# Performance work log

Hardware: AMD Instinct MI355X
Metric: run time of the kernel (lower is better)

Reference implementation:

```python
import jax, jax.numpy as jnp
import numpy as np

B, NP, P, DIM = 128, 64, 128, 512
DST, DCONV, DEPTH = 16, 4, 2
DIN = 2 * DIM          # expand * dim
DTR = DIM // 16        # dt_rank
NCLS = 32


def setup_inputs() -> dict:
    key = jax.random.key(0)
    ks = jax.random.split(key, 12)
    r = lambda k, shape, s=0.02: jax.random.normal(k, shape, jnp.float32) * s
    A_log = jnp.log(jnp.arange(1, DST + 1, dtype=jnp.float32))  # S4D-real init
    return {
        "series": jax.random.normal(ks[0], (B, NP * P), jnp.float32),
        "seg_w": r(ks[1], (NP, P, DIM)),
        "seg_b": jnp.zeros((NP, DIM), jnp.float32),
        "ln_g": jnp.ones((NP, DIM), jnp.float32),
        "ln_b": jnp.zeros((NP, DIM), jnp.float32),
        "in_proj_w": r(ks[2], (DEPTH, 2 * DIN, DIM)),
        "conv_w": r(ks[3], (DEPTH, DIN, DCONV), 0.1),
        "conv_b": jnp.zeros((DEPTH, DIN), jnp.float32),
        "x_proj_w": r(ks[4], (DEPTH, DTR + 2 * DST, DIN)),
        "dt_proj_w": r(ks[5], (DEPTH, DIN, DTR), 0.1),
        "dt_proj_b": r(ks[6], (DEPTH, DIN), 0.5) - 4.0,  # small softplus(dt)
        "A_log": jnp.tile(A_log, (DEPTH, DIN, 1)),
        "D": jnp.ones((DEPTH, DIN), jnp.float32),
        "out_proj_w": r(ks[7], (DEPTH, DIM, DIN)),
        "head_ln_g": jnp.ones((NP * DIM,), jnp.float32),
        "head_ln_b": jnp.zeros((NP * DIM,), jnp.float32),
        "head_w": r(ks[8], (NCLS, NP * DIM)),
        "head_b": jnp.zeros((NCLS,), jnp.float32),
    }


def _layernorm(x, g, b, eps=1e-5):
    mu = x.mean(-1, keepdims=True)
    var = x.var(-1, keepdims=True)
    return (x - mu) / jnp.sqrt(var + eps) * g + b


def _mamba_block(x, wi, cw, cb, wx, wdt, bdt, A_log, Dp, wo):
    # x: [b, l, DIM]
    b, l, _ = x.shape
    xz = jnp.einsum('bld,ed->ble', x, wi)            # [b, l, 2*DIN]
    u, z = jnp.split(xz, 2, axis=-1)
    # depthwise causal conv1d (kernel DCONV, left pad DCONV-1)
    up = jnp.pad(u, ((0, 0), (DCONV - 1, 0), (0, 0)))
    uc = sum(up[:, k:k + l, :] * cw[:, k] for k in range(DCONV)) + cb
    uc = jax.nn.silu(uc)
    x_dbl = jnp.einsum('bld,ed->ble', uc, wx)        # [b, l, DTR+2*DST]
    dt, Bm, Cm = jnp.split(x_dbl, [DTR, DTR + DST], axis=-1)
    delta = jax.nn.softplus(jnp.einsum('blr,dr->bld', dt, wdt) + bdt)  # [b,l,DIN]
    A = -jnp.exp(A_log)                               # [DIN, DST]

    def step(h, inp):
        d_t, B_t, C_t, u_t = inp                      # [b,DIN],[b,DST],[b,DST],[b,DIN]
        dA = jnp.exp(d_t[:, :, None] * A)             # [b, DIN, DST]
        h = dA * h + (d_t * u_t)[:, :, None] * B_t[:, None, :]
        y = jnp.einsum('bdn,bn->bd', h, C_t)
        return h, y

    xs = (delta.transpose(1, 0, 2), Bm.transpose(1, 0, 2),
          Cm.transpose(1, 0, 2), uc.transpose(1, 0, 2))
    h0 = jnp.zeros((b, DIN, DST), x.dtype)
    _, ys = jax.lax.scan(step, h0, xs)                # [l, b, DIN]
    y = ys.transpose(1, 0, 2) + uc * Dp
    y = y * jax.nn.silu(z)
    return jnp.einsum('bld,ed->ble', y, wo)           # [b, l, DIM]


def _forward(series, seg_w, seg_b, ln_g, ln_b, in_proj_w, conv_w, conv_b,
             x_proj_w, dt_proj_w, dt_proj_b, A_log, D, out_proj_w,
             head_ln_g, head_ln_b, head_w, head_b):
    b = series.shape[0]
    x = series.reshape(b, NP, P)                      # equal-size pathway split
    x = jnp.einsum('bnp,npd->bnd', x, seg_w) + seg_b  # per-pathway Linear
    x = _layernorm(x, ln_g, ln_b)                     # per-pathway LayerNorm
    for i in range(DEPTH):                            # stacked Mamba (no residual)
        x = _mamba_block(x, in_proj_w[i], conv_w[i], conv_b[i], x_proj_w[i],
                         dt_proj_w[i], dt_proj_b[i], A_log[i], D[i], out_proj_w[i])
    x = x.reshape(b, NP * DIM)
    x = _layernorm(x, head_ln_g, head_ln_b)
    return x @ head_w.T + head_b


def reference(series, seg_w, seg_b, ln_g, ln_b, in_proj_w, conv_w, conv_b,
              x_proj_w, dt_proj_w, dt_proj_b, A_log, D, out_proj_w,
              head_ln_g, head_ln_b, head_w, head_b):
    return _forward(series, seg_w, seg_b, ln_g, ln_b, in_proj_w, conv_w, conv_b,
                    x_proj_w, dt_proj_w, dt_proj_b, A_log, D, out_proj_w,
                    head_ln_g, head_ln_b, head_w, head_b)
```

## Files before the change

### kernel.cpp

```cpp
#include <hip/hip_runtime.h>

typedef unsigned short u16;
typedef unsigned int   u32;
typedef __attribute__((ext_vector_type(8))) short short8;
typedef __attribute__((ext_vector_type(4))) float floatx4;

static __device__ __forceinline__ float silu_f(float x){
  return x / (1.f + __expf(-x));
}
static __device__ __forceinline__ float bfu2f(u16 u){
  union { u32 i; float f; } v; v.i = ((u32)u) << 16; return v.f;
}
static __device__ __forceinline__ u16 f2bfu(float f){
  union { float f; u32 i; } v; v.f = f;
  u32 x = v.i;
  u32 r = (x + 0x7fffu + ((x >> 16) & 1u)) >> 16;
  return (u16)r;
}
static __device__ __forceinline__ float softplus_f(float v){
  return fmaxf(v, 0.f) + log1pf(__expf(-fabsf(v)));
}

constexpr int cB = 128, cNP = 64, cP = 128, cDIM = 512, cDIN = 1024;
constexpr int cDST = 16, cDTR = 32, cNCLS = 32;
constexpr int cBL = cB * cNP;
constexpr int cXZ = 2 * cDIN;

__global__ __launch_bounds__(256) void k_f2bf(
    const float* __restrict__ src, u16* __restrict__ dst)
{
  const int i = (blockIdx.x * 256 + threadIdx.x) * 4;
  float4 v = *(const float4*)(src + i);
  ushort4 o;
  o.x = f2bfu(v.x); o.y = f2bfu(v.y); o.z = f2bfu(v.z); o.w = f2bfu(v.w);
  *(ushort4*)(dst + i) = o;
}

__global__ __launch_bounds__(256) void k_segT(
    const float* __restrict__ src, u16* __restrict__ dst)
{
  const int n = blockIdx.z;
  const int p0 = blockIdx.x * 32;
  const int d0 = blockIdx.y * 32;
  const int tx = threadIdx.x & 31;
  const int ty = threadIdx.x >> 5;
  __shared__ float t[32][33];
#pragma unroll
  for (int r = 0; r < 4; ++r)
    t[ty + r * 8][tx] = src[(size_t)n * (cP * cDIM) + (p0 + ty + r * 8) * cDIM + d0 + tx];
  __syncthreads();
#pragma unroll
  for (int r = 0; r < 4; ++r)
    dst[(size_t)n * (cDIM * cP) + (d0 + ty + r * 8) * cP + p0 + tx] =
        f2bfu(t[tx][ty + r * 8]);
}

template<bool AF32, int EPI>
__global__ __launch_bounds__(256) void k_gemm_mfma(
    const void* __restrict__ Av, int lda,
    const u16* __restrict__ W,
    float* __restrict__ C, int ldc,
    u16* __restrict__ Cb, int ldcb,
    const float* __restrict__ bias,
    int K, long azs, long wzs, long czs,
    const float* __restrict__ cwp, const float* __restrict__ cbp,
    u16* __restrict__ ucp)
{
  constexpr int LDT = 40;
  __shared__ __align__(16) u16 As[128 * LDT];
  __shared__ __align__(16) u16 Ws[128 * LDT];
  __shared__ __align__(16) u16 sU[(EPI == 2) ? 128 * 128 : 1];

  const int bz = blockIdx.z;
  const u16* Wz = W + (size_t)bz * wzs;

  const int tid = threadIdx.x;
  const int bm = blockIdx.x * 128;
  const int bn = blockIdx.y * 128;
  const int wave = tid >> 6;
  const int lane = tid & 63;
  const int wm = (wave & 1) * 64;
  const int wn = (wave >> 1) * 64;
  const int l15 = lane & 15;
  const int quad = lane >> 4;

  floatx4 acc[4][4];
#pragma unroll
  for (int i = 0; i < 4; ++i)
#pragma unroll
    for (int j = 0; j < 4; ++j) acc[i][j] = (floatx4){0.f, 0.f, 0.f, 0.f};

  const int r0 = tid >> 2;
  const int c0 = (tid & 3) * 8;

  const float* Af = (const float*)Av + (AF32 ? (size_t)bz * azs : 0);
  const u16*   Ab = (const u16*)Av + (AF32 ? 0 : (size_t)bz * azs);

  float4 fa0, fb0, fa1, fb1;
  short8 ra0, ra1, rw0, rw1;

  if constexpr (AF32) {
    const float* p0 = Af + (size_t)(bm + r0) * lda + c0;
    const float* p1 = Af + (size_t)(bm + r0 + 64) * lda + c0;
    fa0 = *(const float4*)p0; fb0 = *(const float4*)(p0 + 4);
    fa1 = *(const float4*)p1; fb1 = *(const float4*)(p1 + 4);
  } else {
    ra0 = *(const short8*)(Ab + (size_t)(bm + r0)      * lda + c0);
    ra1 = *(const short8*)(Ab + (size_t)(bm + r0 + 64) * lda + c0);
  }
  rw0 = *(const short8*)(Wz + (size_t)(bn + r0)      * K + c0);
  rw1 = *(const short8*)(Wz + (size_t)(bn + r0 + 64) * K + c0);

  for (int k0 = 0; k0 < K; k0 += 32) {
    if constexpr (AF32) {
      short8 s0, s1;
      s0[0] = (short)f2bfu(fa0.x); s0[1] = (short)f2bfu(fa0.y);
      s0[2] = (short)f2bfu(fa0.z); s0[3] = (short)f2bfu(fa0.w);
      s0[4] = (short)f2bfu(fb0.x); s0[5] = (short)f2bfu(fb0.y);
      s0[6] = (short)f2bfu(fb0.z); s0[7] = (short)f2bfu(fb0.w);
      s1[0] = (short)f2bfu(fa1.x); s1[1] = (short)f2bfu(fa1.y);
      s1[2] = (short)f2bfu(fa1.z); s1[3] = (short)f2bfu(fa1.w);
      s1[4] = (short)f2bfu(fb1.x); s1[5] = (short)f2bfu(fb1.y);
      s1[6] = (short)f2bfu(fb1.z); s1[7] = (short)f2bfu(fb1.w);
      *(short8*)&As[r0 * LDT + c0] = s0;
      *(short8*)&As[(r0 + 64) * LDT + c0] = s1;
    } else {
      *(short8*)&As[r0 * LDT + c0] = ra0;
      *(short8*)&As[(r0 + 64) * LDT + c0] = ra1;
    }
    *(short8*)&Ws[r0 * LDT + c0] = rw0;
    *(short8*)&Ws[(r0 + 64) * LDT + c0] = rw1;
    __syncthreads();

    const int kn = k0 + 32;
    if (kn < K) {
      if constexpr (AF32) {
        const float* p0 = Af + (size_t)(bm + r0) * lda + kn + c0;
        const float* p1 = Af + (size_t)(bm + r0 + 64) * lda + kn + c0;
        fa0 = *(const float4*)p0; fb0 = *(const float4*)(p0 + 4);
        fa1 = *(const float4*)p1; fb1 = *(const float4*)(p1 + 4);
      } else {
        ra0 = *(const short8*)(Ab + (size_t)(bm + r0)      * lda + kn + c0);
        ra1 = *(const short8*)(Ab + (size_t)(bm + r0 + 64) * lda + kn + c0);
      }
      rw0 = *(const short8*)(Wz + (size_t)(bn + r0)      * K + kn + c0);
      rw1 = *(const short8*)(Wz + (size_t)(bn + r0 + 64) * K + kn + c0);
    }

    short8 af[4], bf[4];
#pragma unroll
    for (int i = 0; i < 4; ++i)
      af[i] = *(const short8*)&As[(wm + i * 16 + l15) * LDT + quad * 8];
#pragma unroll
    for (int j = 0; j < 4; ++j)
      bf[j] = *(const short8*)&Ws[(wn + j * 16 + l15) * LDT + quad * 8];
#pragma unroll
    for (int i = 0; i < 4; ++i)
#pragma unroll
      for (int j = 0; j < 4; ++j)
        acc[i][j] = __builtin_amdgcn_mfma_f32_16x16x32_bf16(
            af[i], bf[j], acc[i][j], 0, 0, 0);
    __syncthreads();
  }

  if constexpr (EPI == 2) {
    if (bn < cDIN) {
#pragma unroll
      for (int i = 0; i < 4; ++i) {
        const int mi = wm + i * 16 + quad * 4;
#pragma unroll
        for (int j = 0; j < 4; ++j) {
          const int nj = wn + j * 16 + l15;
#pragma unroll
          for (int r = 0; r < 4; ++r)
            sU[(mi + r) * 128 + nj] = f2bfu(acc[i][j][r]);
        }
      }
      __syncthreads();
      const int c = tid & 127;
      const int s = tid >> 7;
      const int b = (bm >> 6) + s;
      const int d = bn + c;
      const float w0 = cwp[d * 4 + 0], w1 = cwp[d * 4 + 1];
      const float w2 = cwp[d * 4 + 2], w3 = cwp[d * 4 + 3];
      const float cbias = cbp[d];
      u16* dst = ucp + (size_t)b * cNP * cDIN + d;
      float u0 = 0.f, u1 = 0.f, u2 = 0.f;
#pragma unroll 8
      for (int l = 0; l < cNP; ++l) {
        float u3 = bfu2f(sU[(s * 64 + l) * 128 + c]);
        float v = w0 * u0 + w1 * u1 + w2 * u2 + w3 * u3 + cbias;
        dst[(size_t)l * cDIN] = f2bfu(silu_f(v));
        u0 = u1; u1 = u2; u2 = u3;
      }
      return;
    }
  }

#pragma unroll
  for (int i = 0; i < 4; ++i) {
    const int m0 = bm + wm + i * 16 + quad * 4;
#pragma unroll
    for (int j = 0; j < 4; ++j) {
      const int n = bn + wn + j * 16 + l15;
      if constexpr (EPI == 1) {
        const float bs = bias[n];
#pragma unroll
        for (int r = 0; r < 4; ++r)
          Cb[(size_t)(m0 + r) * ldcb + n + bz * czs] =
              f2bfu(softplus_f(acc[i][j][r] + bs));
      } else {
        if (C) {
#pragma unroll
          for (int r = 0; r < 4; ++r)
            C[(size_t)(m0 + r) * ldc + n + bz * czs] = acc[i][j][r];
        }
        if (Cb) {
#pragma unroll
          for (int r = 0; r < 4; ++r)
            Cb[(size_t)(m0 + r) * ldcb + n + bz * czs] = f2bfu(acc[i][j][r]);
        }
      }
    }
  }
}

__global__ __launch_bounds__(256) void k_ln(
    const float* __restrict__ xs, const float* __restrict__ sb,
    const float* __restrict__ ln_g, const float* __restrict__ ln_b,
    u16* __restrict__ x0b)
{
  const int tid = threadIdx.x;
  const int r = blockIdx.x * 4 + (tid >> 6);
  const int lane = tid & 63;
  const int d = lane * 8;
  const int n = r & 63;

  const float* row = xs + (size_t)r * cDIM + d;
  float4 a = *(const float4*)row;
  float4 b = *(const float4*)(row + 4);
  const float* sbp = sb + n * cDIM + d;
  float4 s0 = *(const float4*)sbp;
  float4 s1 = *(const float4*)(sbp + 4);
  a.x += s0.x; a.y += s0.y; a.z += s0.z; a.w += s0.w;
  b.x += s1.x; b.y += s1.y; b.z += s1.z; b.w += s1.w;

  float s  = a.x + a.y + a.z + a.w + b.x + b.y + b.z + b.w;
  float s2 = a.x*a.x + a.y*a.y + a.z*a.z + a.w*a.w
           + b.x*b.x + b.y*b.y + b.z*b.z + b.w*b.w;
#pragma unroll
  for (int m = 1; m < 64; m <<= 1) {
    s  += __shfl_xor(s,  m, 64);
    s2 += __shfl_xor(s2, m, 64);
  }
  const float mu = s * (1.f / cDIM);
  const float var = s2 * (1.f / cDIM) - mu * mu;
  const float rstd = rsqrtf(var + 1e-5f);

  const float* g = ln_g + n * cDIM + d;
  const float* be = ln_b + n * cDIM + d;
  float4 g0 = *(const float4*)g, g1 = *(const float4*)(g + 4);
  float4 b0 = *(const float4*)be, b1 = *(const float4*)(be + 4);
  ushort4 o0, o1;
  o0.x = f2bfu((a.x - mu) * rstd * g0.x + b0.x);
  o0.y = f2bfu((a.y - mu) * rstd * g0.y + b0.y);
  o0.z = f2bfu((a.z - mu) * rstd * g0.z + b0.z);
  o0.w = f2bfu((a.w - mu) * rstd * g0.w + b0.w);
  o1.x = f2bfu((b.x - mu) * rstd * g1.x + b1.x);
  o1.y = f2bfu((b.y - mu) * rstd * g1.y + b1.y);
  o1.z = f2bfu((b.z - mu) * rstd * g1.z + b1.z);
  o1.w = f2bfu((b.w - mu) * rstd * g1.w + b1.w);
  *(ushort4*)(x0b + (size_t)r * cDIM + d) = o0;
  *(ushort4*)(x0b + (size_t)r * cDIM + d + 4) = o1;
}

__global__ __launch_bounds__(128) void k_xproj(
    const u16* __restrict__ A, const u16* __restrict__ W,
    float* __restrict__ xpart)
{
  constexpr int LDT = 40;
  __shared__ __align__(16) u16 As[128 * LDT];
  __shared__ __align__(16) u16 Ws[64 * LDT];

  const int tid = threadIdx.x;
  const int bm = blockIdx.x * 128;
  const int kbase = blockIdx.y * 256;
  const int wave = tid >> 6;
  const int lane = tid & 63;
  const int wm = wave * 64;
  const int l15 = lane & 15;
  const int quad = lane >> 4;

  floatx4 acc[4][4];
#pragma unroll
  for (int i = 0; i < 4; ++i)
#pragma unroll
    for (int j = 0; j < 4; ++j) acc[i][j] = (floatx4){0.f, 0.f, 0.f, 0.f};

  short8 rA[4], rW[2];
#pragma unroll
  for (int it = 0; it < 4; ++it) {
    int idx = tid + it * 128, row = idx >> 2, cc = (idx & 3) * 8;
    rA[it] = *(const short8*)(A + (size_t)(bm + row) * cDIN + kbase + cc);
  }
#pragma unroll
  for (int it = 0; it < 2; ++it) {
    int idx = tid + it * 128, row = idx >> 2, cc = (idx & 3) * 8;
    rW[it] = *(const short8*)(W + (size_t)row * cDIN + kbase + cc);
  }

  for (int kk = 0; kk < 256; kk += 32) {
#pragma unroll
    for (int it = 0; it < 4; ++it) {
      int idx = tid + it * 128, row = idx >> 2, cc = (idx & 3) * 8;
      *(short8*)&As[row * LDT + cc] = rA[it];
    }
#pragma unroll
    for (int it = 0; it < 2; ++it) {
      int idx = tid + it * 128, row = idx >> 2, cc = (idx & 3) * 8;
      *(short8*)&Ws[row * LDT + cc] = rW[it];
    }
    __syncthreads();

    if (kk + 32 < 256) {
      const int k0 = kbase + kk + 32;
#pragma unroll
      for (int it = 0; it < 4; ++it) {
        int idx = tid + it * 128, row = idx >> 2, cc = (idx & 3) * 8;
        rA[it] = *(const short8*)(A + (size_t)(bm + row) * cDIN + k0 + cc);
      }
#pragma unroll
      for (int it = 0; it < 2; ++it) {
        int idx = tid + it * 128, row = idx >> 2, cc = (idx & 3) * 8;
        rW[it] = *(const short8*)(W + (size_t)row * cDIN + k0 + cc);
      }
    }

    short8 af[4], bf[4];
#pragma unroll
    for (int i = 0; i < 4; ++i)
      af[i] = *(const short8*)&As[(wm + i * 16 + l15) * LDT + quad * 8];
#pragma unroll
    for (int j = 0; j < 4; ++j)
      bf[j] = *(const short8*)&Ws[(j * 16 + l15) * LDT + quad * 8];
#pragma unroll
    for (int i = 0; i < 4; ++i)
#pragma unroll
      for (int j = 0; j < 4; ++j)
        acc[i][j] = __builtin_amdgcn_mfma_f32_16x16x32_bf16(
            af[i], bf[j], acc[i][j], 0, 0, 0);
    __syncthreads();
  }

  float* out = xpart + (size_t)blockIdx.y * cBL * 64;
#pragma unroll
  for (int i = 0; i < 4; ++i) {
    const int m0 = bm + wm + i * 16 + quad * 4;
#pragma unroll
    for (int j = 0; j < 4; ++j) {
      const int n = j * 16 + l15;
#pragma unroll
      for (int r = 0; r < 4; ++r)
        out[(size_t)(m0 + r) * 64 + n] = acc[i][j][r];
    }
  }
}

__global__ __launch_bounds__(256) void k_xred(
    const float* __restrict__ xpart, float* __restrict__ C,
    u16* __restrict__ Cb)
{
  const int i = (blockIdx.x * 256 + threadIdx.x) * 4;
  float4 s = *(const float4*)(xpart + i);
#pragma unroll
  for (int k = 1; k < 4; ++k) {
    float4 v = *(const float4*)(xpart + (size_t)k * cBL * 64 + i);
    s.x += v.x; s.y += v.y; s.z += v.z; s.w += v.w;
  }
  *(float4*)(C + i) = s;
  ushort4 o;
  o.x = f2bfu(s.x); o.y = f2bfu(s.y); o.z = f2bfu(s.z); o.w = f2bfu(s.w);
  *(ushort4*)(Cb + i) = o;
}

__global__ __launch_bounds__(256) void k_scan(
    const u16* __restrict__ xz16, u16* __restrict__ uc,
    const float* __restrict__ xdbl, const float* __restrict__ A_log,
    const float* __restrict__ Dp)
{
  const int b = blockIdx.x;
  const int tid = threadIdx.x;
  const int d = blockIdx.y * 256 + tid;

  __shared__ float sBC[cNP][32];
  {
    const float4* src = (const float4*)xdbl;
    for (int i = tid; i < cNP * 8; i += 256) {
      int l = i >> 3, q = i & 7;
      *(float4*)&sBC[l][q * 4] = src[(size_t)(b * cNP + l) * 16 + 8 + q];
    }
  }

  float A[cDST];
  {
    const float4* ap = (const float4*)(A_log + (size_t)d * cDST);
#pragma unroll
    for (int q = 0; q < 4; ++q) {
      float4 w = ap[q];
      A[q*4+0] = -__expf(w.x); A[q*4+1] = -__expf(w.y);
      A[q*4+2] = -__expf(w.z); A[q*4+3] = -__expf(w.w);
    }
  }
  const float a1 = A[0];
  bool geom = true;
#pragma unroll
  for (int n = 1; n < cDST; ++n)
    geom = geom && (fabsf(A[n] - (float)(n + 1) * a1) <= 1e-4f * fabsf(A[n]));

  float h[cDST];
#pragma unroll
  for (int n = 0; n < cDST; ++n) h[n] = 0.f;
  const float Dv = Dp[d];
  __syncthreads();

  const u16* dsrc = xz16 + d;
  const u16* zsrc = xz16 + cDIN + d;
  u16* usrc = uc + d;
  const size_t rb = (size_t)b * cNP;

  float dvc[8], zvc[8], uvc[8];
#pragma unroll
  for (int i = 0; i < 8; ++i) {
    dvc[i] = bfu2f(dsrc[(rb + i) * cXZ]);
    zvc[i] = bfu2f(zsrc[(rb + i) * cXZ]);
    uvc[i] = bfu2f(usrc[(rb + i) * cDIN]);
  }

  if (geom) {
    for (int c = 0; c < 8; ++c) {
      float dvn[8], zvn[8], uvn[8];
      if (c < 7) {
#pragma unroll
        for (int i = 0; i < 8; ++i) {
          const size_t row = rb + (c + 1) * 8 + i;
          dvn[i] = bfu2f(dsrc[row * cXZ]);
          zvn[i] = bfu2f(zsrc[row * cXZ]);
          uvn[i] = bfu2f(usrc[row * cDIN]);
        }
      }
      u16 yo[8];
#pragma unroll
      for (int i = 0; i < 8; ++i) {
        const int l = c * 8 + i;
        const float dv = dvc[i], zv = zvc[i], uv = uvc[i];
        const float du = dv * uv;
        const float e1 = __expf(dv * a1);
        float dA = e1;
        float y = 0.f;
#pragma unroll
        for (int n = 0; n < cDST; ++n) {
          h[n] = dA * h[n] + du * sBC[l][n];
          y += h[n] * sBC[l][16 + n];
          dA *= e1;
        }
        y = (y + uv * Dv) * silu_f(zv);
        yo[i] = f2bfu(y);
      }
#pragma unroll
      for (int i = 0; i < 8; ++i)
        usrc[(rb + c * 8 + i) * cDIN] = yo[i];
      if (c < 7) {
#pragma unroll
        for (int i = 0; i < 8; ++i) {
          dvc[i] = dvn[i]; zvc[i] = zvn[i]; uvc[i] = uvn[i];
        }
      }
    }
  } else {
    for (int c = 0; c < 8; ++c) {
      float dvn[8], zvn[8], uvn[8];
      if (c < 7) {
#pragma unroll
        for (int i = 0; i < 8; ++i) {
          const size_t row = rb + (c + 1) * 8 + i;
          dvn[i] = bfu2f(dsrc[row * cXZ]);
          zvn[i] = bfu2f(zsrc[row * cXZ]);
          uvn[i] = bfu2f(usrc[row * cDIN]);
        }
      }
      u16 yo[8];
#pragma unroll
      for (int i = 0; i < 8; ++i) {
        const int l = c * 8 + i;
        const float dv = dvc[i], zv = zvc[i], uv = uvc[i];
        const float du = dv * uv;
        float y = 0.f;
#pragma unroll
        for (int n = 0; n < cDST; ++n) {
          float dA = __expf(dv * A[n]);
          h[n] = dA * h[n] + du * sBC[l][n];
          y += h[n] * sBC[l][16 + n];
        }
        y = (y + uv * Dv) * silu_f(zv);
        yo[i] = f2bfu(y);
      }
#pragma unroll
      for (int i = 0; i < 8; ++i)
        usrc[(rb + c * 8 + i) * cDIN] = yo[i];
      if (c < 7) {
#pragma unroll
        for (int i = 0; i < 8; ++i) {
          dvc[i] = dvn[i]; zvc[i] = zvn[i]; uvc[i] = uvn[i];
        }
      }
    }
  }
}

__global__ __launch_bounds__(256) void k_hstats1(
    const float* __restrict__ x, float* __restrict__ pst)
{
  const int b = blockIdx.x;
  const int chunk = blockIdx.y;
  const int tid = threadIdx.x;
  const float4* r4 = (const float4*)(x + (size_t)b * (cNP * cDIM) + chunk * 4096);
  float4 v = r4[tid];
  float4 w = r4[tid + 256];
  float4 u = r4[tid + 512];
  float4 t = r4[tid + 768];
  float s  = v.x + v.y + v.z + v.w + w.x + w.y + w.z + w.w
           + u.x + u.y + u.z + u.w + t.x + t.y + t.z + t.w;
  float s2 = v.x*v.x + v.y*v.y + v.z*v.z + v.w*v.w
           + w.x*w.x + w.y*w.y + w.z*w.z + w.w*w.w
           + u.x*u.x + u.y*u.y + u.z*u.z + u.w*u.w
           + t.x*t.x + t.y*t.y + t.z*t.z + t.w*t.w;
  __shared__ float red[512];
  red[tid] = s; red[256 + tid] = s2;
  __syncthreads();
  for (int st = 128; st > 0; st >>= 1) {
    if (tid < st) { red[tid] += red[tid + st]; red[256+tid] += red[256+tid+st]; }
    __syncthreads();
  }
  if (tid == 0) {
    pst[(b * 8 + chunk) * 2]     = red[0];
    pst[(b * 8 + chunk) * 2 + 1] = red[256];
  }
}

__global__ __launch_bounds__(128) void k_hstats2(
    const float* __restrict__ pst, float* __restrict__ stats)
{
  const int b = threadIdx.x;
  float s = 0.f, s2 = 0.f;
#pragma unroll
  for (int c = 0; c < 8; ++c) {
    s  += pst[(b * 8 + c) * 2];
    s2 += pst[(b * 8 + c) * 2 + 1];
  }
  const float mu = s * (1.f / (cNP * cDIM));
  const float var = s2 * (1.f / (cNP * cDIM)) - mu * mu;
  stats[2 * b]     = mu;
  stats[2 * b + 1] = rsqrtf(var + 1e-5f);
}

__global__ __launch_bounds__(256) void k_head1(
    const float* __restrict__ x, const float* __restrict__ stats,
    const float* __restrict__ hg, const float* __restrict__ hb,
    const u16* __restrict__ hwb, float* __restrict__ hpart)
{
  const int b = blockIdx.x;
  const int chunk = blockIdx.y;
  const int tid = threadIdx.x;
  const float mu = stats[2 * b], rstd = stats[2 * b + 1];
  const float* row = x + (size_t)b * (cNP * cDIM);
  const int k0 = chunk * 2048;

  float acc[cNCLS];
#pragma unroll
  for (int c = 0; c < cNCLS; ++c) acc[c] = 0.f;

#pragma unroll
  for (int it = 0; it < 4; ++it) {
    const int i0 = k0 + it * 512 + tid * 2;
    float xn0 = (row[i0]     - mu) * rstd * hg[i0]     + hb[i0];
    float xn1 = (row[i0 + 1] - mu) * rstd * hg[i0 + 1] + hb[i0 + 1];
#pragma unroll
    for (int c = 0; c < cNCLS; ++c) {
      u32 w2 = *(const u32*)(hwb + (size_t)c * (cNP * cDIM) + i0);
      acc[c] += xn0 * bfu2f((u16)(w2 & 0xffffu)) + xn1 * bfu2f((u16)(w2 >> 16));
    }
  }

  __shared__ float sred[cNCLS * 257];
#pragma unroll
  for (int c = 0; c < cNCLS; ++c) sred[c * 257 + tid] = acc[c];
  __syncthreads();
  if (tid < cNCLS * 8) {
    const int c = tid >> 3, p = tid & 7;
    float s = 0.f;
#pragma unroll
    for (int i = 0; i < 32; ++i) s += sred[c * 257 + p * 32 + i];
    s += __shfl_xor(s, 1, 64);
    s += __shfl_xor(s, 2, 64);
    s += __shfl_xor(s, 4, 64);
    if (p == 0) hpart[(size_t)(b * 16 + chunk) * cNCLS + c] = s;
  }
}

__global__ __launch_bounds__(64) void k_head2(
    const float* __restrict__ hpart, const float* __restrict__ hbias,
    float* __restrict__ out)
{
  const int b = blockIdx.x;
  const int c = threadIdx.x;
  if (c < cNCLS) {
    float s = 0.f;
#pragma unroll
    for (int k = 0; k < 16; ++k)
      s += hpart[(size_t)(b * 16 + k) * cNCLS + c];
    out[b * cNCLS + c] = s + hbias[c];
  }
}

extern "C" void kernel_launch(void* const* d_in, const int* in_sizes, int n_in,
                              void* d_out, int out_size, void* d_ws, size_t ws_size,
                              hipStream_t stream)
{
  (void)in_sizes; (void)n_in; (void)out_size; (void)ws_size;

  const float* series    = (const float*)d_in[0];
  const float* seg_w     = (const float*)d_in[1];
  const float* seg_b     = (const float*)d_in[2];
  const float* ln_g      = (const float*)d_in[3];
  const float* ln_b      = (const float*)d_in[4];
  const float* in_proj_w = (const float*)d_in[5];
  const float* conv_w    = (const float*)d_in[6];
  const float* conv_b    = (const float*)d_in[7];
  const float* x_proj_w  = (const float*)d_in[8];
  const float* dt_proj_w = (const float*)d_in[9];
  const float* dt_proj_b = (const float*)d_in[10];
  const float* A_log     = (const float*)d_in[11];
  const float* Dp        = (const float*)d_in[12];
  const float* out_proj_w= (const float*)d_in[13];
  const float* head_ln_g = (const float*)d_in[14];
  const float* head_ln_b = (const float*)d_in[15];
  const float* head_w    = (const float*)d_in[16];
  const float* head_b    = (const float*)d_in[17];

  u16*   xz16   = (u16*)d_ws;
  float* x0     = (float*)(xz16 + (size_t)cBL * cXZ);
  float* xsegf  = x0;
  float* xdbl   = x0 + (size_t)cBL * cDIM;
  float* stats  = xdbl + (size_t)cBL * 64;
  float* pst    = stats + 256;
  float* hpart  = pst + 128 * 8 * 2;
  u16*   x0b    = (u16*)(hpart + 128 * 16 * 32);
  u16*   wib    = x0b + (size_t)cBL * cDIM;
  u16*   wob    = wib + (size_t)2 * (2*cDIN) * cDIM;
  u16*   wdtb   = wob + (size_t)2 * cDIM * cDIN;
  u16*   wxb    = wdtb + (size_t)2 * cDIN * cDTR;
  u16*   xdbl16 = wxb + (size_t)2 * 64 * cDIN;
  u16*   wsegT  = xdbl16 + (size_t)cBL * 64;
  u16*   ucb16  = wsegT + (size_t)cNP * cDIM * cP;
  u16*   hwb    = ucb16 + (size_t)cBL * cDIN;
  float* xpart  = (float*)x0b;

  k_f2bf<<<(2 * (2*cDIN) * cDIM) / 1024, 256, 0, stream>>>(in_proj_w, wib);
  k_f2bf<<<(2 * cDIM * cDIN) / 1024, 256, 0, stream>>>(out_proj_w, wob);
  k_f2bf<<<(2 * cDIN * cDTR) / 1024, 256, 0, stream>>>(dt_proj_w, wdtb);
  k_f2bf<<<(2 * 64 * cDIN) / 1024, 256, 0, stream>>>(x_proj_w, wxb);
  k_f2bf<<<(cNCLS * cNP * cDIM) / 1024, 256, 0, stream>>>(head_w, hwb);
  k_segT<<<dim3(cP/32, cDIM/32, cNP), 256, 0, stream>>>(seg_w, wsegT);

  k_gemm_mfma<true,0><<<dim3(1, cDIM/128, cNP), 256, 0, stream>>>(
      series, cNP * cP, wsegT, xsegf, cNP * cDIM, (u16*)nullptr, 0,
      nullptr, cP, (long)cP, (long)cDIM * cP, (long)cDIM,
      nullptr, nullptr, nullptr);
  k_ln<<<cBL / 4, 256, 0, stream>>>(xsegf, seg_b, ln_g, ln_b, x0b);

  for (int dep = 0; dep < 2; ++dep) {
    const u16*   wi  = wib  + (size_t)dep * (2*cDIN) * cDIM;
    const u16*   wo  = wob  + (size_t)dep * cDIM * cDIN;
    const u16*   wdt = wdtb + (size_t)dep * cDIN * cDTR;
    const u16*   wx  = wxb  + (size_t)dep * 64 * cDIN;
    const float* cwd = conv_w     + (size_t)dep * cDIN * 4;
    const float* cbd = conv_b     + (size_t)dep * cDIN;
    const float* bdt = dt_proj_b  + (size_t)dep * cDIN;
    const float* Ald = A_log      + (size_t)dep * cDIN * cDST;
    const float* Dd  = Dp         + (size_t)dep * cDIN;

    k_gemm_mfma<false,2><<<dim3(cBL/128, (2*cDIN)/128), 256, 0, stream>>>(
        x0b, cDIM, wi, (float*)nullptr, 0, xz16, cXZ, nullptr, cDIM, 0, 0, 0,
        cwd, cbd, ucb16);
    k_xproj<<<dim3(cBL / 128, 4), 128, 0, stream>>>(ucb16, wx, xpart);
    k_xred<<<(cBL * 64) / 1024, 256, 0, stream>>>(xpart, xdbl, xdbl16);
    k_gemm_mfma<false,1><<<dim3(cBL/128, cDIN/128), 256, 0, stream>>>(
        xdbl16, 64, wdt, (float*)nullptr, 0, xz16, cXZ, bdt, cDTR, 0, 0, 0,
        nullptr, nullptr, nullptr);
    k_scan<<<dim3(cB, 4), 256, 0, stream>>>(xz16, ucb16, xdbl, Ald, Dd);
    k_gemm_mfma<false,0><<<dim3(cBL/128, cDIM/128), 256, 0, stream>>>(
        ucb16, cDIN, wo,
        dep ? x0 : (float*)nullptr, cDIM,
        dep ? (u16*)nullptr : x0b, cDIM,
        nullptr, cDIN, 0, 0, 0,
        nullptr, nullptr, nullptr);
  }

  k_hstats1<<<dim3(cB, 8), 256, 0, stream>>>(x0, pst);
  k_hstats2<<<1, 128, 0, stream>>>(pst, stats);
  k_head1<<<dim3(cB, 16), 256, 0, stream>>>(x0, stats, head_ln_g, head_ln_b,
                                            hwb, hpart);
  k_head2<<<cB, 64, 0, stream>>>(hpart, head_b, (float*)d_out);
}
```

Before: 401.2 us.

## Fuse x_proj split-K reduction into consumers, merge weight casts, unroll scan

Removes the separate split-K reduction kernel for x_proj. The dt_proj GEMM (new AMODE 2) and the scan kernel now each sum the four fp32 partials directly when loading. The five weight-cast launches become one multi-segment kernel. The scan inner loop gets four independent accumulators and a power-chained dA to shorten dependency chains. In exchange, partials are re-read redundantly by each dt_proj column block and by each scan block, and the bf16 rounding point for dt changes slightly.

```diff
diff --git a/kernel.cpp b/kernel.cpp
--- a/kernel.cpp
+++ b/kernel.cpp
@@ -25,15 +25,40 @@
 constexpr int cDST = 16, cDTR = 32, cNCLS = 32;
 constexpr int cBL = cB * cNP;
 constexpr int cXZ = 2 * cDIN;
-
-__global__ __launch_bounds__(256) void k_f2bf(
-    const float* __restrict__ src, u16* __restrict__ dst)
-{
-  const int i = (blockIdx.x * 256 + threadIdx.x) * 4;
-  float4 v = *(const float4*)(src + i);
+constexpr long cPSTR = (long)cBL * 64;
+
+__global__ __launch_bounds__(256) void k_f2bf_all(
+    const float* __restrict__ s0, u16* __restrict__ d0, int n0,
+    const float* __restrict__ s1, u16* __restrict__ d1, int n1,
+    const float* __restrict__ s2, u16* __restrict__ d2, int n2,
+    const float* __restrict__ s3, u16* __restrict__ d3, int n3,
+    const float* __restrict__ s4, u16* __restrict__ d4, int n4)
+{
+  int i = blockIdx.x * 256 + threadIdx.x;
+  const float* s; u16* d;
+  if (i < n0) { s = s0; d = d0; }
+  else {
+    i -= n0;
+    if (i < n1) { s = s1; d = d1; }
+    else {
+      i -= n1;
+      if (i < n2) { s = s2; d = d2; }
+      else {
+        i -= n2;
+        if (i < n3) { s = s3; d = d3; }
+        else {
+          i -= n3;
+          if (i >= n4) return;
+          s = s4; d = d4;
+        }
+      }
+    }
+  }
+  const size_t off = (size_t)i * 4;
+  float4 v = *(const float4*)(s + off);
   ushort4 o;
   o.x = f2bfu(v.x); o.y = f2bfu(v.y); o.z = f2bfu(v.z); o.w = f2bfu(v.w);
-  *(ushort4*)(dst + i) = o;
+  *(ushort4*)(d + off) = o;
 }
 
 __global__ __launch_bounds__(256) void k_segT(
@@ -55,7 +80,7 @@
         f2bfu(t[tx][ty + r * 8]);
 }
 
-template<bool AF32, int EPI>
+template<int AMODE, int EPI>
 __global__ __launch_bounds__(256) void k_gemm_mfma(
     const void* __restrict__ Av, int lda,
     const u16* __restrict__ W,
@@ -93,18 +118,18 @@
   const int r0 = tid >> 2;
   const int c0 = (tid & 3) * 8;
 
-  const float* Af = (const float*)Av + (AF32 ? (size_t)bz * azs : 0);
-  const u16*   Ab = (const u16*)Av + (AF32 ? 0 : (size_t)bz * azs);
+  const float* Af = (const float*)Av + (AMODE == 1 ? (size_t)bz * azs : 0);
+  const u16*   Ab = (const u16*)Av + (AMODE == 0 ? (size_t)bz * azs : 0);
 
   float4 fa0, fb0, fa1, fb1;
   short8 ra0, ra1, rw0, rw1;
 
-  if constexpr (AF32) {
+  if constexpr (AMODE == 1) {
     const float* p0 = Af + (size_t)(bm + r0) * lda + c0;
     const float* p1 = Af + (size_t)(bm + r0 + 64) * lda + c0;
     fa0 = *(const float4*)p0; fb0 = *(const float4*)(p0 + 4);
     fa1 = *(const float4*)p1; fb1 = *(const float4*)(p1 + 4);
-  } else {
+  } else if constexpr (AMODE == 0) {
     ra0 = *(const short8*)(Ab + (size_t)(bm + r0)      * lda + c0);
     ra1 = *(const short8*)(Ab + (size_t)(bm + r0 + 64) * lda + c0);
   }
@@ -112,7 +137,7 @@
   rw1 = *(const short8*)(Wz + (size_t)(bn + r0 + 64) * K + c0);
 
   for (int k0 = 0; k0 < K; k0 += 32) {
-    if constexpr (AF32) {
+    if constexpr (AMODE == 1) {
       short8 s0, s1;
       s0[0] = (short)f2bfu(fa0.x); s0[1] = (short)f2bfu(fa0.y);
       s0[2] = (short)f2bfu(fa0.z); s0[3] = (short)f2bfu(fa0.w);
@@ -124,9 +149,30 @@
       s1[6] = (short)f2bfu(fb1.z); s1[7] = (short)f2bfu(fb1.w);
       *(short8*)&As[r0 * LDT + c0] = s0;
       *(short8*)&As[(r0 + 64) * LDT + c0] = s1;
-    } else {
+    } else if constexpr (AMODE == 0) {
       *(short8*)&As[r0 * LDT + c0] = ra0;
       *(short8*)&As[(r0 + 64) * LDT + c0] = ra1;
+    } else {
+      const float* base = (const float*)Av;
+#pragma unroll
+      for (int h = 0; h < 2; ++h) {
+        const float* p = base + (size_t)(bm + r0 + h * 64) * 64 + c0;
+        float4 a = *(const float4*)p;
+        float4 b = *(const float4*)(p + 4);
+#pragma unroll
+        for (int kc = 1; kc < 4; ++kc) {
+          const float* q = p + (size_t)kc * azs;
+          float4 va = *(const float4*)q, vb = *(const float4*)(q + 4);
+          a.x += va.x; a.y += va.y; a.z += va.z; a.w += va.w;
+          b.x += vb.x; b.y += vb.y; b.z += vb.z; b.w += vb.w;
+        }
+        short8 st;
+        st[0] = (short)f2bfu(a.x); st[1] = (short)f2bfu(a.y);
+        st[2] = (short)f2bfu(a.z); st[3] = (short)f2bfu(a.w);
+        st[4] = (short)f2bfu(b.x); st[5] = (short)f2bfu(b.y);
+        st[6] = (short)f2bfu(b.z); st[7] = (short)f2bfu(b.w);
+        *(short8*)&As[(r0 + h * 64) * LDT + c0] = st;
+      }
     }
     *(short8*)&Ws[r0 * LDT + c0] = rw0;
     *(short8*)&Ws[(r0 + 64) * LDT + c0] = rw1;
@@ -134,12 +180,12 @@
 
     const int kn = k0 + 32;
     if (kn < K) {
-      if constexpr (AF32) {
+      if constexpr (AMODE == 1) {
         const float* p0 = Af + (size_t)(bm + r0) * lda + kn + c0;
         const float* p1 = Af + (size_t)(bm + r0 + 64) * lda + kn + c0;
         fa0 = *(const float4*)p0; fb0 = *(const float4*)(p0 + 4);
         fa1 = *(const float4*)p1; fb1 = *(const float4*)(p1 + 4);
-      } else {
+      } else if constexpr (AMODE == 0) {
         ra0 = *(const short8*)(Ab + (size_t)(bm + r0)      * lda + kn + c0);
         ra1 = *(const short8*)(Ab + (size_t)(bm + r0 + 64) * lda + kn + c0);
       }
@@ -352,7 +398,7 @@
     __syncthreads();
   }
 
-  float* out = xpart + (size_t)blockIdx.y * cBL * 64;
+  float* out = xpart + (size_t)blockIdx.y * cPSTR;
 #pragma unroll
   for (int i = 0; i < 4; ++i) {
     const int m0 = bm + wm + i * 16 + quad * 4;
@@ -366,26 +412,9 @@
   }
 }
 
-__global__ __launch_bounds__(256) void k_xred(
-    const float* __restrict__ xpart, float* __restrict__ C,
-    u16* __restrict__ Cb)
-{
-  const int i = (blockIdx.x * 256 + threadIdx.x) * 4;
-  float4 s = *(const float4*)(xpart + i);
-#pragma unroll
-  for (int k = 1; k < 4; ++k) {
-    float4 v = *(const float4*)(xpart + (size_t)k * cBL * 64 + i);
-    s.x += v.x; s.y += v.y; s.z += v.z; s.w += v.w;
-  }
-  *(float4*)(C + i) = s;
-  ushort4 o;
-  o.x = f2bfu(s.x); o.y = f2bfu(s.y); o.z = f2bfu(s.z); o.w = f2bfu(s.w);
-  *(ushort4*)(Cb + i) = o;
-}
-
 __global__ __launch_bounds__(256) void k_scan(
     const u16* __restrict__ xz16, u16* __restrict__ uc,
-    const float* __restrict__ xdbl, const float* __restrict__ A_log,
+    const float* __restrict__ xpart, const float* __restrict__ A_log,
     const float* __restrict__ Dp)
 {
   const int b = blockIdx.x;
@@ -394,10 +423,16 @@
 
   __shared__ float sBC[cNP][32];
   {
-    const float4* src = (const float4*)xdbl;
     for (int i = tid; i < cNP * 8; i += 256) {
       int l = i >> 3, q = i & 7;
-      *(float4*)&sBC[l][q * 4] = src[(size_t)(b * cNP + l) * 16 + 8 + q];
+      const float* p = xpart + (size_t)(b * cNP + l) * 64 + 32 + q * 4;
+      float4 s = *(const float4*)p;
+#pragma unroll
+      for (int kc = 1; kc < 4; ++kc) {
+        float4 v = *(const float4*)(p + (size_t)kc * cPSTR);
+        s.x += v.x; s.y += v.y; s.z += v.z; s.w += v.w;
+      }
+      *(float4*)&sBC[l][q * 4] = s;
     }
   }
 
@@ -455,14 +490,24 @@
         const float dv = dvc[i], zv = zvc[i], uv = uvc[i];
         const float du = dv * uv;
         const float e1 = __expf(dv * a1);
-        float dA = e1;
-        float y = 0.f;
-#pragma unroll
-        for (int n = 0; n < cDST; ++n) {
-          h[n] = dA * h[n] + du * sBC[l][n];
-          y += h[n] * sBC[l][16 + n];
-          dA *= e1;
-        }
+        const float e2 = e1 * e1;
+        const float e4 = e2 * e2;
+        float p0 = e1, p1 = e2, p2 = e2 * e1, p3 = e4;
+        float y0 = 0.f, y1 = 0.f, y2 = 0.f, y3 = 0.f;
+#pragma unroll
+        for (int g = 0; g < 4; ++g) {
+          const int n = g * 4;
+          h[n+0] = p0 * h[n+0] + du * sBC[l][n+0];
+          y0 += h[n+0] * sBC[l][16 + n+0];
+          h[n+1] = p1 * h[n+1] + du * sBC[l][n+1];
+          y1 += h[n+1] * sBC[l][16 + n+1];
+          h[n+2] = p2 * h[n+2] + du * sBC[l][n+2];
+          y2 += h[n+2] * sBC[l][16 + n+2];
+          h[n+3] = p3 * h[n+3] + du * sBC[l][n+3];
+          y3 += h[n+3] * sBC[l][16 + n+3];
+          if (g < 3) { p0 *= e4; p1 *= e4; p2 *= e4; p3 *= e4; }
+        }
+        float y = (y0 + y1) + (y2 + y3);
         y = (y + uv * Dv) * silu_f(zv);
         yo[i] = f2bfu(y);
       }
@@ -494,13 +539,23 @@
         const int l = c * 8 + i;
         const float dv = dvc[i], zv = zvc[i], uv = uvc[i];
         const float du = dv * uv;
-        float y = 0.f;
-#pragma unroll
-        for (int n = 0; n < cDST; ++n) {
-          float dA = __expf(dv * A[n]);
-          h[n] = dA * h[n] + du * sBC[l][n];
-          y += h[n] * sBC[l][16 + n];
-        }
+        float y0 = 0.f, y1 = 0.f, y2 = 0.f, y3 = 0.f;
+#pragma unroll
+        for (int n = 0; n < cDST; n += 4) {
+          float dA0 = __expf(dv * A[n+0]);
+          float dA1 = __expf(dv * A[n+1]);
+          float dA2 = __expf(dv * A[n+2]);
+          float dA3 = __expf(dv * A[n+3]);
+          h[n+0] = dA0 * h[n+0] + du * sBC[l][n+0];
+          y0 += h[n+0] * sBC[l][16 + n+0];
+          h[n+1] = dA1 * h[n+1] + du * sBC[l][n+1];
+          y1 += h[n+1] * sBC[l][16 + n+1];
+          h[n+2] = dA2 * h[n+2] + du * sBC[l][n+2];
+          y2 += h[n+2] * sBC[l][16 + n+2];
+          h[n+3] = dA3 * h[n+3] + du * sBC[l][n+3];
+          y3 += h[n+3] * sBC[l][16 + n+3];
+        }
+        float y = (y0 + y1) + (y2 + y3);
         y = (y + uv * Dv) * silu_f(zv);
         yo[i] = f2bfu(y);
       }
@@ -650,8 +705,7 @@
   u16*   xz16   = (u16*)d_ws;
   float* x0     = (float*)(xz16 + (size_t)cBL * cXZ);
   float* xsegf  = x0;
-  float* xdbl   = x0 + (size_t)cBL * cDIM;
-  float* stats  = xdbl + (size_t)cBL * 64;
+  float* stats  = x0 + (size_t)cBL * cDIM;
   float* pst    = stats + 256;
   float* hpart  = pst + 128 * 8 * 2;
   u16*   x0b    = (u16*)(hpart + 128 * 16 * 32);
@@ -659,20 +713,20 @@
   u16*   wob    = wib + (size_t)2 * (2*cDIN) * cDIM;
   u16*   wdtb   = wob + (size_t)2 * cDIM * cDIN;
   u16*   wxb    = wdtb + (size_t)2 * cDIN * cDTR;
-  u16*   xdbl16 = wxb + (size_t)2 * 64 * cDIN;
-  u16*   wsegT  = xdbl16 + (size_t)cBL * 64;
+  u16*   wsegT  = wxb + (size_t)2 * 64 * cDIN;
   u16*   ucb16  = wsegT + (size_t)cNP * cDIM * cP;
   u16*   hwb    = ucb16 + (size_t)cBL * cDIN;
   float* xpart  = (float*)x0b;
 
-  k_f2bf<<<(2 * (2*cDIN) * cDIM) / 1024, 256, 0, stream>>>(in_proj_w, wib);
-  k_f2bf<<<(2 * cDIM * cDIN) / 1024, 256, 0, stream>>>(out_proj_w, wob);
-  k_f2bf<<<(2 * cDIN * cDTR) / 1024, 256, 0, stream>>>(dt_proj_w, wdtb);
-  k_f2bf<<<(2 * 64 * cDIN) / 1024, 256, 0, stream>>>(x_proj_w, wxb);
-  k_f2bf<<<(cNCLS * cNP * cDIM) / 1024, 256, 0, stream>>>(head_w, hwb);
+  k_f2bf_all<<<4288, 256, 0, stream>>>(
+      in_proj_w,  wib,  (2 * (2*cDIN) * cDIM) / 4,
+      out_proj_w, wob,  (2 * cDIM * cDIN) / 4,
+      dt_proj_w,  wdtb, (2 * cDIN * cDTR) / 4,
+      x_proj_w,   wxb,  (2 * 64 * cDIN) / 4,
+      head_w,     hwb,  (cNCLS * cNP * cDIM) / 4);
   k_segT<<<dim3(cP/32, cDIM/32, cNP), 256, 0, stream>>>(seg_w, wsegT);
 
-  k_gemm_mfma<true,0><<<dim3(1, cDIM/128, cNP), 256, 0, stream>>>(
+  k_gemm_mfma<1,0><<<dim3(1, cDIM/128, cNP), 256, 0, stream>>>(
       series, cNP * cP, wsegT, xsegf, cNP * cDIM, (u16*)nullptr, 0,
       nullptr, cP, (long)cP, (long)cDIM * cP, (long)cDIM,
       nullptr, nullptr, nullptr);
@@ -689,16 +743,15 @@
     const float* Ald = A_log      + (size_t)dep * cDIN * cDST;
     const float* Dd  = Dp         + (size_t)dep * cDIN;
 
-    k_gemm_mfma<false,2><<<dim3(cBL/128, (2*cDIN)/128), 256, 0, stream>>>(
+    k_gemm_mfma<0,2><<<dim3(cBL/128, (2*cDIN)/128), 256, 0, stream>>>(
         x0b, cDIM, wi, (float*)nullptr, 0, xz16, cXZ, nullptr, cDIM, 0, 0, 0,
         cwd, cbd, ucb16);
     k_xproj<<<dim3(cBL / 128, 4), 128, 0, stream>>>(ucb16, wx, xpart);
-    k_xred<<<(cBL * 64) / 1024, 256, 0, stream>>>(xpart, xdbl, xdbl16);
-    k_gemm_mfma<false,1><<<dim3(cBL/128, cDIN/128), 256, 0, stream>>>(
-        xdbl16, 64, wdt, (float*)nullptr, 0, xz16, cXZ, bdt, cDTR, 0, 0, 0,
-        nullptr, nullptr, nullptr);
-    k_scan<<<dim3(cB, 4), 256, 0, stream>>>(xz16, ucb16, xdbl, Ald, Dd);
-    k_gemm_mfma<false,0><<<dim3(cBL/128, cDIM/128), 256, 0, stream>>>(
+    k_gemm_mfma<2,1><<<dim3(cBL/128, cDIN/128), 256, 0, stream>>>(
+        xpart, 64, wdt, (float*)nullptr, 0, xz16, cXZ, bdt, cDTR,
+        cPSTR, 0, 0, nullptr, nullptr, nullptr);
+    k_scan<<<dim3(cB, 4), 256, 0, stream>>>(xz16, ucb16, xpart, Ald, Dd);
+    k_gemm_mfma<0,0><<<dim3(cBL/128, cDIM/128), 256, 0, stream>>>(
         ucb16, cDIN, wo,
         dep ? x0 : (float*)nullptr, cDIM,
         dep ? (u16*)nullptr : x0b, cDIM,
```

New measurement: 398.1 us. Within noise of the previous version (-0.8%).
